# Optimization experiments

Measured on AMD Instinct MI355X. Metric: run time of the kernel, lower is better.

Reference implementation:

```python
import jax, jax.numpy as jnp
import numpy as np

K = 3
NUM_INTERVALS = 16
INPUT_DIM = 64
OUTPUT_DIM = 64
BATCH = 65536


def make_grid():
    g = jnp.linspace(-1.0, 1.0, NUM_INTERVALS + 1)
    # extended grid as in setup(): repeat first/last k knots
    return jnp.concatenate([g[:K], g, g[-K:]])  # (NUM_INTERVALS + 1 + 2K,)


def setup_inputs() -> dict:
    key = jax.random.key(0)
    k1, k2 = jax.random.split(key)
    x = jax.random.normal(k1, (BATCH, INPUT_DIM), dtype=jnp.float32)
    grid = make_grid().astype(jnp.float32)
    n_coef = grid.shape[0] - K - 1  # = NUM_INTERVALS + K = 19
    coefficients = 0.01 * jax.random.normal(
        k2, (INPUT_DIM, OUTPUT_DIM, n_coef), dtype=jnp.float32
    )
    wb = jnp.ones((OUTPUT_DIM,), jnp.float32)
    ws = jnp.ones((OUTPUT_DIM,), jnp.float32)
    return {"x": x, "coefficients": coefficients, "wb": wb, "ws": ws, "grid": grid}


def _bspline_basis(x, grid, k=K):
    # x: (N, D); grid: (G,). Vectorized over all input dims at once
    # (the original loops over input_dim; math is identical).
    g = grid[None, None, :]        # (1, 1, G)
    xe = x[:, :, None]             # (N, D, 1)
    basis = ((xe >= g[..., :-1]) & (xe < g[..., 1:])).astype(x.dtype)  # (N, D, G-1)

    def safe_div(a, b):
        return a / (b + 1e-5)

    for KK in range(1, k + 1):  # Cox-de Boor recursion (k fixed, small)
        left = safe_div(xe - g[..., :-(KK + 1)], g[..., KK:-1] - g[..., :-(KK + 1)])
        right = safe_div(g[..., KK + 1:] - xe, g[..., KK + 1:] - g[..., 1:-KK])
        basis = left * basis[..., :-1] + right * basis[..., 1:]
    return basis  # (N, D, G-k-1)


def reference(x, coefficients, wb, ws, grid):
    x = jnp.atleast_2d(x)
    # global min-max normalization to [-1, 1] as in __call__
    x = (x - jnp.min(x)) / (jnp.max(x) - jnp.min(x) + 1e-6) * 2 - 1
    x = jnp.clip(x, -1.0, 1.0)
    basis = _bspline_basis(x, grid)  # (N, D, C)
    # sum over input dims of basis @ coefficients[i].T
    spline_result = jnp.einsum("ndc,doc->no", basis, coefficients)  # (N, O)
    # silu(x) @ ones(D, O) == row-sum of silu(x) broadcast across O
    silu_sum = jnp.sum(x * jax.nn.sigmoid(x), axis=1, keepdims=True)  # (N, 1)
    silu_result = silu_sum * jnp.ones((1, OUTPUT_DIM), x.dtype)
    return wb * silu_result + ws * spline_result
```

## Files before the change

kernel.cpp:

```cpp
#include <hip/hip_runtime.h>

typedef __attribute__((ext_vector_type(8))) short short8;
typedef __attribute__((ext_vector_type(4))) float f32x4;

#define NC     19
#define DIM    64
#define ODIM   64
#define NROWS  65536
#define CPAD   24
#define DCH    4
#define NCHUNK (DIM / DCH)
#define KSC    3

#define MM_OFF  0
#define BPLANE  (NCHUNK * KSC * 4 * 64 * 16)
#define BH_OFF  1024
#define BL_OFF  (BH_OFF + BPLANE)

__host__ __device__ constexpr float Gc(int i) {
    int j = (i < 3) ? i : (i < 20 ? i - 3 : i - 6);
    return -1.0f + 0.125f * (float)j;
}
__host__ __device__ constexpr float invLd(int KK, int j) { return 1.0f / (Gc(j + KK) - Gc(j) + 1e-5f); }
__host__ __device__ constexpr float invRd(int KK, int j) { return 1.0f / (Gc(j + KK + 1) - Gc(j + 1) + 1e-5f); }

__device__ __forceinline__ unsigned short bf16_rne(float f) {
    unsigned u = __float_as_uint(f);
    unsigned r = u + 0x7FFFu + ((u >> 16) & 1u);
    return (unsigned short)(r >> 16);
}
__device__ __forceinline__ float bf16_tof(unsigned short h) {
    return __uint_as_float(((unsigned)h) << 16);
}

__device__ __forceinline__ unsigned fenc(float f) {
    unsigned u = __float_as_uint(f);
    return (u & 0x80000000u) ? ~u : (u | 0x80000000u);
}
__device__ __forceinline__ float fdec(unsigned e) {
    unsigned u = (e & 0x80000000u) ? (e & 0x7fffffffu) : ~e;
    return __uint_as_float(u);
}

__device__ __forceinline__ void dense_basis(float x, float* b3) {
    float b0[22];
    #pragma unroll
    for (int j = 0; j < 22; ++j)
        b0[j] = (x >= Gc(j) && x < Gc(j + 1)) ? 1.0f : 0.0f;
    float b1[21];
    #pragma unroll
    for (int j = 0; j < 21; ++j)
        b1[j] = (x - Gc(j)) * invLd(1, j) * b0[j] + (Gc(j + 2) - x) * invRd(1, j) * b0[j + 1];
    float b2[20];
    #pragma unroll
    for (int j = 0; j < 20; ++j)
        b2[j] = (x - Gc(j)) * invLd(2, j) * b1[j] + (Gc(j + 3) - x) * invRd(2, j) * b1[j + 1];
    #pragma unroll
    for (int j = 0; j < 19; ++j)
        b3[j] = (x - Gc(j)) * invLd(3, j) * b2[j] + (Gc(j + 4) - x) * invRd(3, j) * b2[j + 1];
}

__global__ void kan_init(unsigned* mm) {
    mm[0] = 0xFFFFFFFFu;
    mm[1] = 0u;
}

__global__ __launch_bounds__(256) void kan_minmax(const float* __restrict__ x,
                                                  unsigned* __restrict__ mm) {
    const int n4 = (NROWS * DIM) / 4;
    int i0 = blockIdx.x * blockDim.x + threadIdx.x;
    float lmin = 3.0e38f, lmax = -3.0e38f;
    for (int i = i0; i < n4; i += gridDim.x * blockDim.x) {
        float4 v = reinterpret_cast<const float4*>(x)[i];
        lmin = fminf(lmin, fminf(fminf(v.x, v.y), fminf(v.z, v.w)));
        lmax = fmaxf(lmax, fmaxf(fmaxf(v.x, v.y), fmaxf(v.z, v.w)));
    }
    #pragma unroll
    for (int s = 32; s; s >>= 1) {
        lmin = fminf(lmin, __shfl_xor(lmin, s, 64));
        lmax = fmaxf(lmax, __shfl_xor(lmax, s, 64));
    }
    __shared__ float smn[4], smx[4];
    int wv = threadIdx.x >> 6;
    if ((threadIdx.x & 63) == 0) { smn[wv] = lmin; smx[wv] = lmax; }
    __syncthreads();
    if (threadIdx.x == 0) {
        float a = smn[0], b = smx[0];
        #pragma unroll
        for (int k = 1; k < 4; ++k) { a = fminf(a, smn[k]); b = fmaxf(b, smx[k]); }
        atomicMin(&mm[0], fenc(a));
        atomicMax(&mm[1], fenc(b));
    }
}

__global__ __launch_bounds__(256) void kan_tcoef(const float* __restrict__ coef,
                                                 short8* __restrict__ wsBh,
                                                 short8* __restrict__ wsBl) {
    int v = blockIdx.x * 256 + threadIdx.x;
    int ch = v / 768, rem = v - ch * 768;
    int ksl = rem >> 8, rem2 = rem & 255;
    int nf = rem2 >> 6, l = rem2 & 63;
    int o = nf * 16 + (l & 15);
    short8 vh, vl;
    #pragma unroll
    for (int i = 0; i < 8; ++i) {
        int k = ch * 96 + ksl * 32 + (l >> 4) * 8 + i;
        int d = k / CPAD, c = k - d * CPAD;
        float val = (c < NC) ? coef[((size_t)d * ODIM + o) * NC + c] : 0.0f;
        unsigned short hb = bf16_rne(val);
        float lof = val - bf16_tof(hb);
        vh[i] = (short)hb;
        vl[i] = (short)bf16_rne(lof);
    }
    wsBh[v] = vh;
    wsBl[v] = vl;
}

__global__ __launch_bounds__(256, 3) void kan_main(const float* __restrict__ x,
                                                   const char* __restrict__ wsB,
                                                   const float* __restrict__ wb,
                                                   const float* __restrict__ wsp,
                                                   float* __restrict__ out,
                                                   const unsigned* __restrict__ mm) {
    __shared__ short8 sAh[4 * KSC * 4 * 17];
    __shared__ short8 sAl[4 * KSC * 4 * 17];
    __shared__ short8 sBh[KSC * 4 * 64];
    __shared__ short8 sBl[KSC * 4 * 64];
    __shared__ float  sSilu[64];

    const int tid = threadIdx.x;
    const int l   = tid & 63;
    const int w   = tid >> 6;
    const int n0  = blockIdx.x * 64;

    const float mn  = fdec(mm[0]);
    const float mx  = fdec(mm[1]);
    const float den = (mx - mn) + 1e-6f;
    const float inv = 1.0f / den;

    {
        int r16 = l >> 2, q = l & 3;
        int row = n0 + w * 16 + r16;
        const float4* xr = reinterpret_cast<const float4*>(x + (size_t)row * DIM + q * 16);
        float s = 0.0f;
        #pragma unroll
        for (int j = 0; j < 4; ++j) {
            float4 v = xr[j];
            #pragma unroll
            for (int e = 0; e < 4; ++e) {
                float xv = (e == 0) ? v.x : (e == 1) ? v.y : (e == 2) ? v.z : v.w;
                float xn = ((xv - mn) * inv) * 2.0f - 1.0f;
                xn = fminf(fmaxf(xn, -1.0f), 1.0f);
                s += xn * (1.0f / (1.0f + expf(-xn)));
            }
        }
        s += __shfl_xor(s, 1);
        s += __shfl_xor(s, 2);
        if (q == 0) sSilu[w * 16 + r16] = s;
    }

    f32x4 acc[4];
    #pragma unroll
    for (int nf = 0; nf < 4; ++nf) acc[nf] = (f32x4){0.0f, 0.0f, 0.0f, 0.0f};

    const char* pBh = wsB + BH_OFF - BH_OFF;
    const char* pBl = wsB + BPLANE;

    for (int ch = 0; ch < NCHUNK; ++ch) {
        __syncthreads();

        #pragma unroll
        for (int j = 0; j < 3; ++j) {
            int seg = w * 3 + j;
            __builtin_amdgcn_global_load_lds(
                (const __attribute__((address_space(1))) void*)(pBh + (size_t)ch * 12288 + seg * 1024 + l * 16),
                (__attribute__((address_space(3))) void*)((char*)sBh + seg * 1024), 16, 0, 0);
            __builtin_amdgcn_global_load_lds(
                (const __attribute__((address_space(1))) void*)(pBl + (size_t)ch * 12288 + seg * 1024 + l * 16),
                (__attribute__((address_space(3))) void*)((char*)sBl + seg * 1024), 16, 0, 0);
        }

        {
            int r16 = l >> 2;
            int dloc = l & 3;
            int row = n0 + w * 16 + r16;
            float xv = x[(size_t)row * DIM + ch * DCH + dloc];
            float xn = ((xv - mn) * inv) * 2.0f - 1.0f;
            xn = fminf(fmaxf(xn, -1.0f), 1.0f);
            float b3[NC];
            dense_basis(xn, b3);
            #pragma unroll
            for (int cg = 0; cg < 3; ++cg) {
                short8 vh, vl;
                #pragma unroll
                for (int i = 0; i < 8; ++i) {
                    int c = cg * 8 + i;
                    float bv = (c < NC) ? b3[c] : 0.0f;
                    unsigned short hb = bf16_rne(bv);
                    float lof = bv - bf16_tof(hb);
                    vh[i] = (short)hb;
                    vl[i] = (short)bf16_rne(lof);
                }
                int k0 = dloc * CPAD + cg * 8;
                int ksl = k0 >> 5, kg = (k0 & 31) >> 3;
                int slot = ((w * KSC + ksl) * 4 + kg) * 17 + r16;
                sAh[slot] = vh;
                sAl[slot] = vl;
            }
        }

        __syncthreads();

        const int kgc = l >> 4, r16c = l & 15;
        #pragma unroll
        for (int ks = 0; ks < KSC; ++ks) {
            int aslot = ((w * KSC + ks) * 4 + kgc) * 17 + r16c;
            short8 ah = sAh[aslot];
            short8 al = sAl[aslot];
            #pragma unroll
            for (int nf = 0; nf < 4; ++nf) {
                short8 bh = sBh[(ks * 4 + nf) * 64 + l];
                short8 bl = sBl[(ks * 4 + nf) * 64 + l];
                acc[nf] = __builtin_amdgcn_mfma_f32_16x16x32_bf16(ah, bh, acc[nf], 0, 0, 0);
                acc[nf] = __builtin_amdgcn_mfma_f32_16x16x32_bf16(al, bh, acc[nf], 0, 0, 0);
                acc[nf] = __builtin_amdgcn_mfma_f32_16x16x32_bf16(ah, bl, acc[nf], 0, 0, 0);
            }
        }
    }

    #pragma unroll
    for (int nf = 0; nf < 4; ++nf) {
        int o = nf * 16 + (l & 15);
        float wbv = wb[o];
        float wsv = wsp[o];
        #pragma unroll
        for (int v = 0; v < 4; ++v) {
            int rloc = (l >> 4) * 4 + v;
            int row = n0 + w * 16 + rloc;
            out[(size_t)row * ODIM + o] = wbv * sSilu[w * 16 + rloc] + wsv * acc[nf][v];
        }
    }
}

extern "C" void kernel_launch(void* const* d_in, const int* in_sizes, int n_in,
                              void* d_out, int out_size, void* d_ws, size_t ws_size,
                              hipStream_t stream) {
    const float* x    = (const float*)d_in[0];
    const float* coef = (const float*)d_in[1];
    const float* wb   = (const float*)d_in[2];
    const float* wsp  = (const float*)d_in[3];
    float* outp       = (float*)d_out;

    char* ws = (char*)d_ws;
    unsigned* mm  = (unsigned*)(ws + MM_OFF);
    short8* wsBh  = (short8*)(ws + BH_OFF);
    short8* wsBl  = (short8*)(ws + BL_OFF);

    kan_init  <<<1,    1,   0, stream>>>(mm);
    kan_minmax<<<2048, 256, 0, stream>>>(x, mm);
    kan_tcoef <<<48,   256, 0, stream>>>(coef, wsBh, wsBl);
    kan_main  <<<NROWS / 64, 256, 0, stream>>>(x, (const char*)(ws + BH_OFF), wb, wsp, outp, mm);
}
```

Baseline: 208.2 us.

## Replace dense Cox-de Boor with per-interval cubic polynomial tables and larger row tiles

Precomputes, in double precision, cubic polynomial coefficients for the six nonzero B-spline bases on each grid interval, so the main kernel evaluates only six Horner polynomials per element instead of the full recursion. The sparse values are packed into the split-bf16 A tiles in LDS with zero fill. Each block now processes 128 rows, with two M-fragments per wave. B fragments are loaded directly from global memory instead of being staged in LDS, which removes the per-chunk barriers. The init and coefficient-transform kernels are merged into one launch. The risks are extra register pressure and global load latency on B, plus small numerical differences from the polynomial fit.

Measured after the change: 189.4 us. 1.1x faster.

```diff
diff --git a/kernel.cpp b/kernel.cpp
--- a/kernel.cpp
+++ b/kernel.cpp
@@ -4,25 +4,20 @@
 typedef __attribute__((ext_vector_type(4))) float f32x4;
 
 #define NC     19
+#define CPAD   24
 #define DIM    64
 #define ODIM   64
 #define NROWS  65536
-#define CPAD   24
-#define DCH    4
-#define NCHUNK (DIM / DCH)
-#define KSC    3
-
-#define MM_OFF  0
-#define BPLANE  (NCHUNK * KSC * 4 * 64 * 16)
-#define BH_OFF  1024
-#define BL_OFF  (BH_OFF + BPLANE)
+
+#define MM_OFF 0
+#define T_OFF  64
+#define B_OFF  2048
+#define BPLANE (16 * 3 * 4 * 64 * 16)
 
 __host__ __device__ constexpr float Gc(int i) {
     int j = (i < 3) ? i : (i < 20 ? i - 3 : i - 6);
     return -1.0f + 0.125f * (float)j;
 }
-__host__ __device__ constexpr float invLd(int KK, int j) { return 1.0f / (Gc(j + KK) - Gc(j) + 1e-5f); }
-__host__ __device__ constexpr float invRd(int KK, int j) { return 1.0f / (Gc(j + KK + 1) - Gc(j + 1) + 1e-5f); }
 
 __device__ __forceinline__ unsigned short bf16_rne(float f) {
     unsigned u = __float_as_uint(f);
@@ -32,7 +27,6 @@
 __device__ __forceinline__ float bf16_tof(unsigned short h) {
     return __uint_as_float(((unsigned)h) << 16);
 }
-
 __device__ __forceinline__ unsigned fenc(float f) {
     unsigned u = __float_as_uint(f);
     return (u & 0x80000000u) ? ~u : (u | 0x80000000u);
@@ -42,27 +36,85 @@
     return __uint_as_float(u);
 }
 
-__device__ __forceinline__ void dense_basis(float x, float* b3) {
-    float b0[22];
+__device__ void dense_basis_f64(double x, double* b3) {
+    double b0[22];
     #pragma unroll
     for (int j = 0; j < 22; ++j)
-        b0[j] = (x >= Gc(j) && x < Gc(j + 1)) ? 1.0f : 0.0f;
-    float b1[21];
-    #pragma unroll
-    for (int j = 0; j < 21; ++j)
-        b1[j] = (x - Gc(j)) * invLd(1, j) * b0[j] + (Gc(j + 2) - x) * invRd(1, j) * b0[j + 1];
-    float b2[20];
-    #pragma unroll
-    for (int j = 0; j < 20; ++j)
-        b2[j] = (x - Gc(j)) * invLd(2, j) * b1[j] + (Gc(j + 3) - x) * invRd(2, j) * b1[j + 1];
-    #pragma unroll
-    for (int j = 0; j < 19; ++j)
-        b3[j] = (x - Gc(j)) * invLd(3, j) * b2[j] + (Gc(j + 4) - x) * invRd(3, j) * b2[j + 1];
-}
-
-__global__ void kan_init(unsigned* mm) {
-    mm[0] = 0xFFFFFFFFu;
-    mm[1] = 0u;
+        b0[j] = (x >= (double)Gc(j) && x < (double)Gc(j + 1)) ? 1.0 : 0.0;
+    double b1[21];
+    #pragma unroll
+    for (int j = 0; j < 21; ++j) {
+        float dl = (Gc(j + 1) - Gc(j)) + 1e-5f;
+        float dr = (Gc(j + 2) - Gc(j + 1)) + 1e-5f;
+        b1[j] = (x - (double)Gc(j)) / (double)dl * b0[j] + ((double)Gc(j + 2) - x) / (double)dr * b0[j + 1];
+    }
+    double b2[20];
+    #pragma unroll
+    for (int j = 0; j < 20; ++j) {
+        float dl = (Gc(j + 2) - Gc(j)) + 1e-5f;
+        float dr = (Gc(j + 3) - Gc(j + 1)) + 1e-5f;
+        b2[j] = (x - (double)Gc(j)) / (double)dl * b1[j] + ((double)Gc(j + 3) - x) / (double)dr * b1[j + 1];
+    }
+    #pragma unroll
+    for (int j = 0; j < 19; ++j) {
+        float dl = (Gc(j + 3) - Gc(j)) + 1e-5f;
+        float dr = (Gc(j + 4) - Gc(j + 1)) + 1e-5f;
+        b3[j] = (x - (double)Gc(j)) / (double)dl * b2[j] + ((double)Gc(j + 4) - x) / (double)dr * b2[j + 1];
+    }
+}
+
+__global__ __launch_bounds__(256) void kan_prep(const float* __restrict__ coef,
+                                                short8* __restrict__ wsBh,
+                                                short8* __restrict__ wsBl,
+                                                float4* __restrict__ wsT,
+                                                unsigned* __restrict__ mm) {
+    const int tid = threadIdx.x;
+    if (blockIdx.x < 48) {
+        int v = blockIdx.x * 256 + tid;
+        int ch = v / 768, rem = v - ch * 768;
+        int ksl = rem >> 8, rem2 = rem & 255;
+        int nf = rem2 >> 6, l = rem2 & 63;
+        int o = nf * 16 + (l & 15);
+        short8 vh, vl;
+        #pragma unroll
+        for (int i = 0; i < 8; ++i) {
+            int k = ch * 96 + ksl * 32 + (l >> 4) * 8 + i;
+            int d = k / CPAD, c = k - d * CPAD;
+            float val = (c < NC) ? coef[((size_t)d * ODIM + o) * NC + c] : 0.0f;
+            unsigned short hb = bf16_rne(val);
+            float lof = val - bf16_tof(hb);
+            vh[i] = (short)hb;
+            vl[i] = (short)bf16_rne(lof);
+        }
+        wsBh[v] = vh;
+        wsBl[v] = vl;
+    } else {
+        if (tid == 0) { mm[0] = 0xFFFFFFFFu; mm[1] = 0u; }
+        if (tid < 96) {
+            int m = tid / 6, j = tid % 6;
+            int w0 = min(max(m - 1, 0), 13);
+            double knot = -1.0 + 0.125 * (double)m;
+            const double S[4] = {0.125, 0.375, 0.625, 0.875};
+            double y[4];
+            #pragma unroll
+            for (int i = 0; i < 4; ++i) {
+                double b3[19];
+                dense_basis_f64(knot + 0.125 * S[i], b3);
+                y[i] = b3[w0 + j];
+            }
+            double d01 = (y[1] - y[0]) / (S[1] - S[0]);
+            double d12 = (y[2] - y[1]) / (S[2] - S[1]);
+            double d23 = (y[3] - y[2]) / (S[3] - S[2]);
+            double d012 = (d12 - d01) / (S[2] - S[0]);
+            double d123 = (d23 - d12) / (S[3] - S[1]);
+            double d0123 = (d123 - d012) / (S[3] - S[0]);
+            double a3 = d0123;
+            double a2 = d012 - d0123 * (S[0] + S[1] + S[2]);
+            double a1 = d01 - d012 * (S[0] + S[1]) + d0123 * (S[0]*S[1] + S[0]*S[2] + S[1]*S[2]);
+            double a0 = y[0] - d01 * S[0] + d012 * S[0]*S[1] - d0123 * S[0]*S[1]*S[2];
+            wsT[tid] = make_float4((float)a0, (float)a1, (float)a2, (float)a3);
+        }
+    }
 }
 
 __global__ __launch_bounds__(256) void kan_minmax(const float* __restrict__ x,
@@ -93,59 +145,39 @@
     }
 }
 
-__global__ __launch_bounds__(256) void kan_tcoef(const float* __restrict__ coef,
-                                                 short8* __restrict__ wsBh,
-                                                 short8* __restrict__ wsBl) {
-    int v = blockIdx.x * 256 + threadIdx.x;
-    int ch = v / 768, rem = v - ch * 768;
-    int ksl = rem >> 8, rem2 = rem & 255;
-    int nf = rem2 >> 6, l = rem2 & 63;
-    int o = nf * 16 + (l & 15);
-    short8 vh, vl;
-    #pragma unroll
-    for (int i = 0; i < 8; ++i) {
-        int k = ch * 96 + ksl * 32 + (l >> 4) * 8 + i;
-        int d = k / CPAD, c = k - d * CPAD;
-        float val = (c < NC) ? coef[((size_t)d * ODIM + o) * NC + c] : 0.0f;
-        unsigned short hb = bf16_rne(val);
-        float lof = val - bf16_tof(hb);
-        vh[i] = (short)hb;
-        vl[i] = (short)bf16_rne(lof);
-    }
-    wsBh[v] = vh;
-    wsBl[v] = vl;
-}
-
 __global__ __launch_bounds__(256, 3) void kan_main(const float* __restrict__ x,
-                                                   const char* __restrict__ wsB,
+                                                   const short8* __restrict__ wsBh,
+                                                   const short8* __restrict__ wsBl,
+                                                   const float4* __restrict__ wsT,
                                                    const float* __restrict__ wb,
                                                    const float* __restrict__ wsp,
                                                    float* __restrict__ out,
                                                    const unsigned* __restrict__ mm) {
-    __shared__ short8 sAh[4 * KSC * 4 * 17];
-    __shared__ short8 sAl[4 * KSC * 4 * 17];
-    __shared__ short8 sBh[KSC * 4 * 64];
-    __shared__ short8 sBl[KSC * 4 * 64];
-    __shared__ float  sSilu[64];
+    __shared__ short8 sAh[8 * 204];
+    __shared__ short8 sAl[8 * 204];
+    __shared__ float4 sT[96];
+    __shared__ float  sSilu[128];
 
     const int tid = threadIdx.x;
     const int l   = tid & 63;
     const int w   = tid >> 6;
-    const int n0  = blockIdx.x * 64;
+    const int n0  = blockIdx.x * 128;
+
+    if (tid < 96) sT[tid] = wsT[tid];
 
     const float mn  = fdec(mm[0]);
     const float mx  = fdec(mm[1]);
-    const float den = (mx - mn) + 1e-6f;
-    const float inv = 1.0f / den;
-
-    {
+    const float inv = 1.0f / ((mx - mn) + 1e-6f);
+
+    #pragma unroll
+    for (int mf = 0; mf < 2; ++mf) {
         int r16 = l >> 2, q = l & 3;
-        int row = n0 + w * 16 + r16;
+        int row = n0 + w * 32 + mf * 16 + r16;
         const float4* xr = reinterpret_cast<const float4*>(x + (size_t)row * DIM + q * 16);
         float s = 0.0f;
         #pragma unroll
-        for (int j = 0; j < 4; ++j) {
-            float4 v = xr[j];
+        for (int jj = 0; jj < 4; ++jj) {
+            float4 v = xr[jj];
             #pragma unroll
             for (int e = 0; e < 4; ++e) {
                 float xv = (e == 0) ? v.x : (e == 1) ? v.y : (e == 2) ? v.z : v.w;
@@ -156,74 +188,108 @@
         }
         s += __shfl_xor(s, 1);
         s += __shfl_xor(s, 2);
-        if (q == 0) sSilu[w * 16 + r16] = s;
-    }
-
-    f32x4 acc[4];
-    #pragma unroll
-    for (int nf = 0; nf < 4; ++nf) acc[nf] = (f32x4){0.0f, 0.0f, 0.0f, 0.0f};
-
-    const char* pBh = wsB + BH_OFF - BH_OFF;
-    const char* pBl = wsB + BPLANE;
-
-    for (int ch = 0; ch < NCHUNK; ++ch) {
-        __syncthreads();
-
-        #pragma unroll
-        for (int j = 0; j < 3; ++j) {
-            int seg = w * 3 + j;
-            __builtin_amdgcn_global_load_lds(
-                (const __attribute__((address_space(1))) void*)(pBh + (size_t)ch * 12288 + seg * 1024 + l * 16),
-                (__attribute__((address_space(3))) void*)((char*)sBh + seg * 1024), 16, 0, 0);
-            __builtin_amdgcn_global_load_lds(
-                (const __attribute__((address_space(1))) void*)(pBl + (size_t)ch * 12288 + seg * 1024 + l * 16),
-                (__attribute__((address_space(3))) void*)((char*)sBl + seg * 1024), 16, 0, 0);
-        }
-
-        {
-            int r16 = l >> 2;
-            int dloc = l & 3;
-            int row = n0 + w * 16 + r16;
-            float xv = x[(size_t)row * DIM + ch * DCH + dloc];
+        if (q == 0) sSilu[w * 32 + mf * 16 + r16] = s;
+    }
+    __syncthreads();
+
+    f32x4 acc[2][4];
+    #pragma unroll
+    for (int mf = 0; mf < 2; ++mf)
+        #pragma unroll
+        for (int nf = 0; nf < 4; ++nf) acc[mf][nf] = (f32x4){0.0f, 0.0f, 0.0f, 0.0f};
+
+    unsigned* sAhw = (unsigned*)sAh;
+    unsigned* sAlw = (unsigned*)sAl;
+    const int r16 = l >> 2, dloc = l & 3;
+    const int kgc = l >> 4, r16c = l & 15;
+
+    for (int ch = 0; ch < 16; ++ch) {
+        #pragma unroll
+        for (int mf = 0; mf < 2; ++mf) {
+            const int abase = (w * 2 + mf) * 204;
+            int row = n0 + w * 32 + mf * 16 + r16;
+            float xv = x[(size_t)row * DIM + ch * 4 + dloc];
             float xn = ((xv - mn) * inv) * 2.0f - 1.0f;
             xn = fminf(fmaxf(xn, -1.0f), 1.0f);
-            float b3[NC];
-            dense_basis(xn, b3);
-            #pragma unroll
-            for (int cg = 0; cg < 3; ++cg) {
-                short8 vh, vl;
+
+            int m = (int)((xn + 1.0f) * 8.0f);
+            m = min(max(m, 0), 15);
+            float knot = -1.0f + 0.125f * (float)m;
+            if (xn < knot) m -= 1;
+            else if (xn >= knot + 0.125f) m += 1;
+            m = min(max(m, 0), 15);
+            int w0 = min(max(m - 1, 0), 13);
+            float s = (xn - (-1.0f + 0.125f * (float)m)) * 8.0f;
+
+            float b[6];
+            #pragma unroll
+            for (int j = 0; j < 6; ++j) {
+                float4 T = sT[m * 6 + j];
+                b[j] = ((T.w * s + T.z) * s + T.y) * s + T.x;
+            }
+            unsigned short hh[6];
+            unsigned short hl[6];
+            #pragma unroll
+            for (int j = 0; j < 6; ++j) {
+                hh[j] = bf16_rne(b[j]);
+                hl[j] = bf16_rne(b[j] - bf16_tof(hh[j]));
+            }
+            const int e = w0 & 1;
+            const int P0 = w0 >> 1;
+            unsigned short vh[8], vl8[8];
+            #pragma unroll
+            for (int i = 0; i < 8; ++i) {
+                unsigned short a = (i < 6) ? hh[i] : (unsigned short)0;
+                unsigned short bsh = (i >= 1 && i <= 6) ? hh[i - 1] : (unsigned short)0;
+                vh[i] = e ? bsh : a;
+                unsigned short c = (i < 6) ? hl[i] : (unsigned short)0;
+                unsigned short dsh = (i >= 1 && i <= 6) ? hl[i - 1] : (unsigned short)0;
+                vl8[i] = e ? dsh : c;
+            }
+            unsigned dwh[4], dwl[4];
+            #pragma unroll
+            for (int k = 0; k < 4; ++k) {
+                dwh[k] = (unsigned)(unsigned short)vh[2 * k] | ((unsigned)(unsigned short)vh[2 * k + 1] << 16);
+                dwl[k] = (unsigned)(unsigned short)vl8[2 * k] | ((unsigned)(unsigned short)vl8[2 * k + 1] << 16);
+            }
+            const short8 z8 = (short8){0, 0, 0, 0, 0, 0, 0, 0};
+            #pragma unroll
+            for (int gi = 0; gi < 3; ++gi) {
+                int g = dloc * 3 + gi;
+                int slot = abase + ((g >> 2) * 4 + (g & 3)) * 17 + r16;
+                sAh[slot] = z8;
+                sAl[slot] = z8;
+            }
+            #pragma unroll
+            for (int pp = 0; pp < 4; ++pp) {
+                int p = P0 + pp;
+                int g = dloc * 3 + (p >> 2);
+                int slot = abase + ((g >> 2) * 4 + (g & 3)) * 17 + r16;
+                sAhw[slot * 4 + (p & 3)] = dwh[pp];
+                sAlw[slot * 4 + (p & 3)] = dwl[pp];
+            }
+        }
+
+        #pragma unroll
+        for (int ks = 0; ks < 3; ++ks) {
+            short8 bh[4], bl[4];
+            #pragma unroll
+            for (int nf = 0; nf < 4; ++nf) {
+                int bv = ((ch * 3 + ks) * 4 + nf) * 64 + l;
+                bh[nf] = wsBh[bv];
+                bl[nf] = wsBl[bv];
+            }
+            #pragma unroll
+            for (int mf = 0; mf < 2; ++mf) {
+                int slotA = (w * 2 + mf) * 204 + (ks * 4 + kgc) * 17 + r16c;
+                short8 ah = sAh[slotA];
+                short8 al = sAl[slotA];
                 #pragma unroll
-                for (int i = 0; i < 8; ++i) {
-                    int c = cg * 8 + i;
-                    float bv = (c < NC) ? b3[c] : 0.0f;
-                    unsigned short hb = bf16_rne(bv);
-                    float lof = bv - bf16_tof(hb);
-                    vh[i] = (short)hb;
-                    vl[i] = (short)bf16_rne(lof);
+                for (int nf = 0; nf < 4; ++nf) {
+                    acc[mf][nf] = __builtin_amdgcn_mfma_f32_16x16x32_bf16(ah, bh[nf], acc[mf][nf], 0, 0, 0);
+                    acc[mf][nf] = __builtin_amdgcn_mfma_f32_16x16x32_bf16(al, bh[nf], acc[mf][nf], 0, 0, 0);
+                    acc[mf][nf] = __builtin_amdgcn_mfma_f32_16x16x32_bf16(ah, bl[nf], acc[mf][nf], 0, 0, 0);
                 }
-                int k0 = dloc * CPAD + cg * 8;
-                int ksl = k0 >> 5, kg = (k0 & 31) >> 3;
-                int slot = ((w * KSC + ksl) * 4 + kg) * 17 + r16;
-                sAh[slot] = vh;
-                sAl[slot] = vl;
-            }
-        }
-
-        __syncthreads();
-
-        const int kgc = l >> 4, r16c = l & 15;
-        #pragma unroll
-        for (int ks = 0; ks < KSC; ++ks) {
-            int aslot = ((w * KSC + ks) * 4 + kgc) * 17 + r16c;
-            short8 ah = sAh[aslot];
-            short8 al = sAl[aslot];
-            #pragma unroll
-            for (int nf = 0; nf < 4; ++nf) {
-                short8 bh = sBh[(ks * 4 + nf) * 64 + l];
-                short8 bl = sBl[(ks * 4 + nf) * 64 + l];
-                acc[nf] = __builtin_amdgcn_mfma_f32_16x16x32_bf16(ah, bh, acc[nf], 0, 0, 0);
-                acc[nf] = __builtin_amdgcn_mfma_f32_16x16x32_bf16(al, bh, acc[nf], 0, 0, 0);
-                acc[nf] = __builtin_amdgcn_mfma_f32_16x16x32_bf16(ah, bl, acc[nf], 0, 0, 0);
             }
         }
     }
@@ -234,10 +300,13 @@
         float wbv = wb[o];
         float wsv = wsp[o];
         #pragma unroll
-        for (int v = 0; v < 4; ++v) {
-            int rloc = (l >> 4) * 4 + v;
-            int row = n0 + w * 16 + rloc;
-            out[(size_t)row * ODIM + o] = wbv * sSilu[w * 16 + rloc] + wsv * acc[nf][v];
+        for (int mf = 0; mf < 2; ++mf) {
+            #pragma unroll
+            for (int v = 0; v < 4; ++v) {
+                int rloc = mf * 16 + (l >> 4) * 4 + v;
+                int row = n0 + w * 32 + rloc;
+                out[(size_t)row * ODIM + o] = wbv * sSilu[w * 32 + rloc] + wsv * acc[mf][nf][v];
+            }
         }
     }
 }
@@ -253,11 +322,11 @@
 
     char* ws = (char*)d_ws;
     unsigned* mm  = (unsigned*)(ws + MM_OFF);
-    short8* wsBh  = (short8*)(ws + BH_OFF);
-    short8* wsBl  = (short8*)(ws + BL_OFF);
-
-    kan_init  <<<1,    1,   0, stream>>>(mm);
+    float4*  wsT  = (float4*)(ws + T_OFF);
+    short8*  wsBh = (short8*)(ws + B_OFF);
+    short8*  wsBl = (short8*)(ws + B_OFF + BPLANE);
+
+    kan_prep  <<<49,   256, 0, stream>>>(coef, wsBh, wsBl, wsT, mm);
     kan_minmax<<<2048, 256, 0, stream>>>(x, mm);
-    kan_tcoef <<<48,   256, 0, stream>>>(coef, wsBh, wsBl);
-    kan_main  <<<NROWS / 64, 256, 0, stream>>>(x, (const char*)(ws + BH_OFF), wb, wsp, outp, mm);
-}
+    kan_main  <<<NROWS / 128, 256, 0, stream>>>(x, wsBh, wsBl, wsT, wb, wsp, outp, mm);
+}
```
